# Performance work log

Hardware: AMD Instinct MI355X
Metric: run time of the kernel (lower is better)

The kernel has to match this reference:

```python
import jax, jax.numpy as jnp
import numpy as np

B, H, L, CHUNK, D = 2, 8, 32, 64, 64
MAX_REL = 32
N = L * CHUNK


def setup_inputs() -> dict:
    key = jax.random.key(0)
    k1, k2, k3 = jax.random.split(key, 3)
    x = jax.random.normal(k1, (B, H, N, D), dtype=jnp.float32)
    pos = jax.random.randint(k2, (B, L, L), 0, 64, dtype=jnp.int64)
    # xavier_uniform-like init for the embeddings table
    table_shape = (2 * MAX_REL + 1, D)
    limit = np.sqrt(6.0 / (table_shape[0] + table_shape[1])).astype(np.float32)
    embeddings_table = jax.random.uniform(
        k3, table_shape, dtype=jnp.float32, minval=-limit, maxval=limit)
    return {"x": x, "pos": pos, "embeddings_table": embeddings_table,
            "chunk_size": CHUNK}


def reference(x, pos, embeddings_table, chunk_size):
    # x: [b,h,N,d], pos: [b,l,l], embeddings_table: [2*mrp+1, d]
    mrp = (embeddings_table.shape[0] - 1) // 2
    idx = jnp.clip(pos, -mrp, mrp) + mrp            # [b,l,l]
    emb = embeddings_table[idx]                      # [b,l,l,d] gather
    b, h, n_tot, d = x.shape
    l = pos.shape[1]
    n = chunk_size
    assert n_tot == l * n
    # '(l n)' split: l outer blocks, n inner positions
    xc = x.reshape(b, h, l, n, d)                    # [b,h,q,n,d]
    # per-chunk dot products: row block q, col block k, row offset n
    scores = jnp.einsum('bhqnd,bqkd->bhqnk', xc, emb)  # [b,h,l,n,l]
    # broadcast over inner column offset m (value independent of m)
    out = jnp.broadcast_to(scores[..., None], (b, h, l, n, l, n))
    return out.reshape(b, h, n_tot, n_tot)           # [b,h,N,N]
```

## Files before the change

kernel.cpp:

```cpp
#include <hip/hip_runtime.h>

#define BB 2
#define HH 8
#define LL 32
#define CHK 64
#define DD 64
#define MAX_REL 32
#define NN 2048
#define RPB 16

__global__ __launch_bounds__(256) void relpos_kernel(
    const float* __restrict__ x,
    const int*   __restrict__ pos,
    const float* __restrict__ table,
    float*       __restrict__ out)
{
    const int blk = blockIdx.x;
    const int sub = blk & 3;
    const int q   = (blk >> 2) & (LL - 1);
    const int bh  = blk >> 7;
    const int b   = bh >> 3;

    const int t    = threadIdx.x;
    const int k    = t >> 3;
    const int part = t & 7;

    int p = pos[(b * LL + q) * LL + k];
    p = min(max(p, -MAX_REL), MAX_REL) + MAX_REL;
    const float* erow = table + (size_t)p * DD + part * 8;
    const float4 ea = *(const float4*)(erow);
    const float4 eb = *(const float4*)(erow + 4);

    __shared__ float sk[RPB][32];

    const int row0 = (bh << 11) + (q << 6) + (sub << 4);
    const float* xbase = x + (size_t)row0 * DD + part * 8;

    #pragma unroll 4
    for (int r = 0; r < RPB; ++r) {
        const float4 xa = *(const float4*)(xbase + (size_t)r * DD);
        const float4 xb = *(const float4*)(xbase + (size_t)r * DD + 4);
        float s = xa.x * ea.x + xa.y * ea.y + xa.z * ea.z + xa.w * ea.w
                + xb.x * eb.x + xb.y * eb.y + xb.z * eb.z + xb.w * eb.w;
        s += __shfl_xor(s, 1);
        s += __shfl_xor(s, 2);
        s += __shfl_xor(s, 4);
        if (part == 0) sk[r][k] = s;
    }
    __syncthreads();

    const int k0 = t >> 4;
    float4* obase = (float4*)(out + (size_t)row0 * NN);
    #pragma unroll
    for (int r = 0; r < RPB; ++r) {
        const float v0 = sk[r][k0];
        const float v1 = sk[r][16 + k0];
        float4* orow = obase + (size_t)r * (NN / 4);
        orow[t]       = make_float4(v0, v0, v0, v0);
        orow[t + 256] = make_float4(v1, v1, v1, v1);
    }
}

extern "C" void kernel_launch(void* const* d_in, const int* in_sizes, int n_in,
                              void* d_out, int out_size, void* d_ws, size_t ws_size,
                              hipStream_t stream) {
    const float* x     = (const float*)d_in[0];
    const int*   pos   = (const int*)d_in[1];
    const float* table = (const float*)d_in[2];
    float*       out   = (float*)d_out;

    dim3 grid(BB * HH * LL * (CHK / RPB));
    relpos_kernel<<<grid, 256, 0, stream>>>(x, pos, table, out);
}
```

Before: 54.37 us.

## Split score computation and broadcast write into two kernels via workspace

Splits the fused kernel in two. The first kernel computes the per-row/per-block scores into a workspace buffer, and the second streams out the broadcast output rows with a wave-per-row layout. The aim is to decouple the small compute phase from the large write-bound phase so each has its own parallelism and no block-level barrier. In exchange it adds a second launch and a round trip through global memory for the scores, and keeps the fused kernel as a fallback when the workspace is too small.

```diff
diff --git a/kernel.cpp b/kernel.cpp
--- a/kernel.cpp
+++ b/kernel.cpp
@@ -7,13 +7,16 @@
 #define DD 64
 #define MAX_REL 32
 #define NN 2048
+#define NROWS (BB * HH * NN)
 #define RPB 16
 
-__global__ __launch_bounds__(256) void relpos_kernel(
+typedef float f32x4 __attribute__((ext_vector_type(4)));
+
+__global__ __launch_bounds__(256) void score_kernel(
     const float* __restrict__ x,
     const int*   __restrict__ pos,
     const float* __restrict__ table,
-    float*       __restrict__ out)
+    float*       __restrict__ sc)
 {
     const int blk = blockIdx.x;
     const int sub = blk & 3;
@@ -28,18 +31,78 @@
     int p = pos[(b * LL + q) * LL + k];
     p = min(max(p, -MAX_REL), MAX_REL) + MAX_REL;
     const float* erow = table + (size_t)p * DD + part * 8;
-    const float4 ea = *(const float4*)(erow);
-    const float4 eb = *(const float4*)(erow + 4);
-
-    __shared__ float sk[RPB][32];
+    const f32x4 ea = *(const f32x4*)(erow);
+    const f32x4 eb = *(const f32x4*)(erow + 4);
 
     const int row0 = (bh << 11) + (q << 6) + (sub << 4);
     const float* xbase = x + (size_t)row0 * DD + part * 8;
 
     #pragma unroll 4
     for (int r = 0; r < RPB; ++r) {
-        const float4 xa = *(const float4*)(xbase + (size_t)r * DD);
-        const float4 xb = *(const float4*)(xbase + (size_t)r * DD + 4);
+        const f32x4 xa = *(const f32x4*)(xbase + (size_t)r * DD);
+        const f32x4 xb = *(const f32x4*)(xbase + (size_t)r * DD + 4);
+        float s = xa.x * ea.x + xa.y * ea.y + xa.z * ea.z + xa.w * ea.w
+                + xb.x * eb.x + xb.y * eb.y + xb.z * eb.z + xb.w * eb.w;
+        s += __shfl_xor(s, 1);
+        s += __shfl_xor(s, 2);
+        s += __shfl_xor(s, 4);
+        if (part == 0) sc[(size_t)(row0 + r) * 32 + k] = s;
+    }
+}
+
+__global__ __launch_bounds__(256) void bcast_kernel(
+    const float* __restrict__ sc,
+    float*       __restrict__ out)
+{
+    const int wid  = blockIdx.x * 4 + (threadIdx.x >> 6);
+    const int lane = threadIdx.x & 63;
+    const int g    = lane >> 4;
+
+    #pragma unroll
+    for (int i = 0; i < 2; ++i) {
+        const int row = wid * 2 + i;
+        const float* srow = sc + (size_t)row * 32;
+        float v[8];
+        #pragma unroll
+        for (int j = 0; j < 8; ++j)
+            v[j] = srow[4 * j + g];
+
+        f32x4* orow = (f32x4*)(out + (size_t)row * NN);
+        #pragma unroll
+        for (int j = 0; j < 8; ++j) {
+            f32x4 v4 = {v[j], v[j], v[j], v[j]};
+            orow[j * 64 + lane] = v4;
+        }
+    }
+}
+
+__global__ __launch_bounds__(256) void relpos_fused(
+    const float* __restrict__ x, const int* __restrict__ pos,
+    const float* __restrict__ table, float* __restrict__ out)
+{
+    const int blk = blockIdx.x;
+    const int sub = blk & 3;
+    const int q   = (blk >> 2) & (LL - 1);
+    const int bh  = blk >> 7;
+    const int b   = bh >> 3;
+    const int t    = threadIdx.x;
+    const int k    = t >> 3;
+    const int part = t & 7;
+
+    int p = pos[(b * LL + q) * LL + k];
+    p = min(max(p, -MAX_REL), MAX_REL) + MAX_REL;
+    const float* erow = table + (size_t)p * DD + part * 8;
+    const f32x4 ea = *(const f32x4*)(erow);
+    const f32x4 eb = *(const f32x4*)(erow + 4);
+
+    __shared__ float sk[RPB][32];
+    const int row0 = (bh << 11) + (q << 6) + (sub << 4);
+    const float* xbase = x + (size_t)row0 * DD + part * 8;
+
+    #pragma unroll 4
+    for (int r = 0; r < RPB; ++r) {
+        const f32x4 xa = *(const f32x4*)(xbase + (size_t)r * DD);
+        const f32x4 xb = *(const f32x4*)(xbase + (size_t)r * DD + 4);
         float s = xa.x * ea.x + xa.y * ea.y + xa.z * ea.z + xa.w * ea.w
                 + xb.x * eb.x + xb.y * eb.y + xb.z * eb.z + xb.w * eb.w;
         s += __shfl_xor(s, 1);
@@ -50,14 +113,14 @@
     __syncthreads();
 
     const int k0 = t >> 4;
-    float4* obase = (float4*)(out + (size_t)row0 * NN);
+    f32x4* obase = (f32x4*)(out + (size_t)row0 * NN);
     #pragma unroll
     for (int r = 0; r < RPB; ++r) {
         const float v0 = sk[r][k0];
         const float v1 = sk[r][16 + k0];
-        float4* orow = obase + (size_t)r * (NN / 4);
-        orow[t]       = make_float4(v0, v0, v0, v0);
-        orow[t + 256] = make_float4(v1, v1, v1, v1);
+        f32x4* orow = obase + (size_t)r * (NN / 4);
+        orow[t]       = (f32x4){v0, v0, v0, v0};
+        orow[t + 256] = (f32x4){v1, v1, v1, v1};
     }
 }
 
@@ -69,6 +132,11 @@
     const float* table = (const float*)d_in[2];
     float*       out   = (float*)d_out;
 
-    dim3 grid(BB * HH * LL * (CHK / RPB));
-    relpos_kernel<<<grid, 256, 0, stream>>>(x, pos, table, out);
+    if (ws_size >= (size_t)NROWS * 32 * sizeof(float)) {
+        float* sc = (float*)d_ws;
+        score_kernel<<<dim3(NROWS / RPB), 256, 0, stream>>>(x, pos, table, sc);
+        bcast_kernel<<<dim3(NROWS / 2 / 4), 256, 0, stream>>>(sc, out);
+    } else {
+        relpos_fused<<<dim3(NROWS / RPB), 256, 0, stream>>>(x, pos, table, out);
+    }
 }
```

Result: slower. 59.40 us (+9.2%).
